# Optimization experiments

Measured on AMD Instinct MI355X. Metric: run time of the kernel, lower is better.

The kernel has to match this reference:

```python
import jax, jax.numpy as jnp
import numpy as np

N, A, C = 65536, 512, 1000


def setup_inputs() -> dict:
    key = jax.random.key(0)
    k1, k2, k3, k4, k5 = jax.random.split(key, 5)
    return {
        "features": jax.random.normal(k1, (N, A), dtype=jnp.float32),
        "labels": jax.random.randint(k2, (N,), 0, C),
        "count": jax.random.uniform(k3, (C,), dtype=jnp.float32) * 100.0,
        "mean": jax.random.normal(k4, (C, A), dtype=jnp.float32),
        "cov": jax.random.uniform(k5, (C, A), dtype=jnp.float32),
    }


def reference(features, labels, count, mean, cov):
    # Per-class counts and feature sums via segment reduction (math identical to
    # the torch onehot-expand NxCxA construction, but O(N*A) instead of O(N*C*A)).
    c = count.shape[0]
    ones = jnp.ones((features.shape[0],), dtype=features.dtype)
    n_c = jax.ops.segment_sum(ones, labels, num_segments=c)            # [C]
    sums = jax.ops.segment_sum(features, labels, num_segments=c)      # [C, A]
    amt = jnp.where(n_c == 0, 1.0, n_c)                                # Amount_CxA (zeros -> 1)
    ave = sums / amt[:, None]                                          # ave_CxA
    diff = features - ave[labels]                                      # onehot*(x - ave) per row
    var = jax.ops.segment_sum(diff * diff, labels, num_segments=c) / amt[:, None]
    # EMA blend weight; torch sets NaN (0/0) entries to 0.
    denom = n_c + count
    w = jnp.where(denom == 0, 0.0, n_c / jnp.where(denom == 0, 1.0, denom))[:, None]  # [C,1]
    cov_new = cov * (1.0 - w) + var * w + w * (1.0 - w) * (mean - ave) ** 2
    mean_new = mean * (1.0 - w) + ave * w
    count_new = count + n_c
    return cov_new, mean_new, count_new
```

## Files before the change

kernel.cpp:

```cpp
#include <hip/hip_runtime.h>
#include <hip/hip_bf16.h>

constexpr int N_ROWS = 65536;
constexpr int N_FEAT = 512;
constexpr int N_FEAT2 = N_FEAT / 2;
constexpr int N_CLS  = 1000;
constexpr int CLS_PAD = 1024;


__global__ void hist_kernel(const int* __restrict__ labels, int* __restrict__ nc, int n) {
    int i = blockIdx.x * blockDim.x + threadIdx.x;
    if (i < n) atomicAdd(&nc[labels[i]], 1);
}

__global__ void scan_kernel(const int* __restrict__ nc,
                            int* __restrict__ offs, int* __restrict__ cursor) {
    __shared__ int tmp[CLS_PAD];
    int t = threadIdx.x;
    int v = (t < N_CLS) ? nc[t] : 0;
    tmp[t] = v;
    __syncthreads();
    for (int d = 1; d < CLS_PAD; d <<= 1) {
        int x = (t >= d) ? tmp[t - d] : 0;
        __syncthreads();
        tmp[t] += x;
        __syncthreads();
    }
    int excl = tmp[t] - v;
    if (t < N_CLS) { offs[t] = excl; cursor[t] = excl; }
}

__global__ void scatter_kernel(const int* __restrict__ labels,
                               int* __restrict__ cursor, int* __restrict__ perm, int n) {
    int i = blockIdx.x * blockDim.x + threadIdx.x;
    if (i < n) {
        int c = labels[i];
        int pos = atomicAdd(&cursor[c], 1);
        perm[pos] = i;
    }
}

__global__ __launch_bounds__(256) void estimator_main(
    const float* __restrict__ features,
    const float* __restrict__ count,
    const float* __restrict__ mean,
    const float* __restrict__ cov,
    const int* __restrict__ nc,
    const int* __restrict__ offs,
    const int* __restrict__ perm,
    float* __restrict__ out) {
    const int c = blockIdx.x;
    const int t = threadIdx.x;
    const int n = nc[c];
    const int start = offs[c];

    __shared__ int lrows[256];
    const float2* __restrict__ f2 = (const float2*)features;

    float sx = 0.f, sy = 0.f, qx = 0.f, qy = 0.f;

    for (int base = 0; base < n; base += 256) {
        int chunk = min(256, n - base);
        __syncthreads();
        if (t < chunk) lrows[t] = perm[start + base + t];
        __syncthreads();
        #pragma unroll 4
        for (int j = 0; j < chunk; ++j) {
            int r = lrows[j];
            float2 v = f2[(size_t)r * N_FEAT2 + t];
            sx += v.x; sy += v.y;
            qx += v.x * v.x; qy += v.y * v.y;
        }
    }

    const float fn  = (float)n;
    const float amt = (n > 0) ? fn : 1.0f;
    const float inv = 1.0f / amt;
    const float avx = sx * inv, avy = sy * inv;
    const float vrx = qx * inv - avx * avx;
    const float vry = qy * inv - avy * avy;

    const float cnt   = count[c];
    const float denom = fn + cnt;
    const float w     = (denom == 0.f) ? 0.f : fn / denom;
    const float omw   = 1.0f - w;

    const float2 mv = ((const float2*)mean)[c * N_FEAT2 + t];
    const float2 cv = ((const float2*)cov)[c * N_FEAT2 + t];
    const float dx = mv.x - avx, dy = mv.y - avy;

    float2 covn, meann;
    covn.x  = cv.x * omw + vrx * w + w * omw * dx * dx;
    covn.y  = cv.y * omw + vry * w + w * omw * dy * dy;
    meann.x = mv.x * omw + avx * w;
    meann.y = mv.y * omw + avy * w;

    float2* outc = (float2*)out;
    float2* outm = (float2*)(out + N_CLS * N_FEAT);
    outc[c * N_FEAT2 + t] = covn;
    outm[c * N_FEAT2 + t] = meann;
    if (t == 0) out[2 * N_CLS * N_FEAT + c] = cnt + fn;
}

extern "C" void kernel_launch(void* const* d_in, const int* in_sizes, int n_in,
                              void* d_out, int out_size, void* d_ws, size_t ws_size,
                              hipStream_t stream) {
    const float* features = (const float*)d_in[0];
    const int*   labels   = (const int*)d_in[1];
    const float* count    = (const float*)d_in[2];
    const float* mean     = (const float*)d_in[3];
    const float* cov      = (const float*)d_in[4];
    float* out = (float*)d_out;

    char* ws = (char*)d_ws;
    int* nc     = (int*)(ws + 0);
    int* offs   = (int*)(ws + 4096);
    int* cursor = (int*)(ws + 8192);
    int* perm   = (int*)(ws + 12288);

    hipMemsetAsync(nc, 0, CLS_PAD * sizeof(int), stream);

    hist_kernel<<<(N_ROWS + 255) / 256, 256, 0, stream>>>(labels, nc, N_ROWS);
    scan_kernel<<<1, CLS_PAD, 0, stream>>>(nc, offs, cursor);
    scatter_kernel<<<(N_ROWS + 255) / 256, 256, 0, stream>>>(labels, cursor, perm, N_ROWS);
    estimator_main<<<N_CLS, 256, 0, stream>>>(features, count, mean, cov,
                                              nc, offs, perm, out);
}
```

Before: 239.5 us.

## Fuse histogram, scan, scatter and estimator into one cooperative kernel

Replaces the memset and four separate kernel launches with a single cooperative kernel that uses grid-wide syncs between the histogram, prefix scan, scatter and per-class reduction phases. The aim is to remove launch overhead and inter-kernel gaps. The trade-off is the cost of four grid barriers, plus the requirement that all 1000 blocks are co-resident; the cooperative launch fails if they are not. The scan now uses 256 threads, each handling four classes.

```diff
diff --git a/kernel.cpp b/kernel.cpp
--- a/kernel.cpp
+++ b/kernel.cpp
@@ -1,72 +1,79 @@
 #include <hip/hip_runtime.h>
-#include <hip/hip_bf16.h>
+#include <hip/hip_cooperative_groups.h>
 
-constexpr int N_ROWS = 65536;
-constexpr int N_FEAT = 512;
+namespace cg = cooperative_groups;
+
+constexpr int N_ROWS  = 65536;
+constexpr int N_FEAT  = 512;
 constexpr int N_FEAT2 = N_FEAT / 2;
-constexpr int N_CLS  = 1000;
-constexpr int CLS_PAD = 1024;
+constexpr int N_CLS   = 1000;
+constexpr int GRID    = 1000;
+constexpr int BLOCK   = 256;
 
 
-__global__ void hist_kernel(const int* __restrict__ labels, int* __restrict__ nc, int n) {
-    int i = blockIdx.x * blockDim.x + threadIdx.x;
-    if (i < n) atomicAdd(&nc[labels[i]], 1);
-}
-
-__global__ void scan_kernel(const int* __restrict__ nc,
-                            int* __restrict__ offs, int* __restrict__ cursor) {
-    __shared__ int tmp[CLS_PAD];
-    int t = threadIdx.x;
-    int v = (t < N_CLS) ? nc[t] : 0;
-    tmp[t] = v;
-    __syncthreads();
-    for (int d = 1; d < CLS_PAD; d <<= 1) {
-        int x = (t >= d) ? tmp[t - d] : 0;
-        __syncthreads();
-        tmp[t] += x;
-        __syncthreads();
-    }
-    int excl = tmp[t] - v;
-    if (t < N_CLS) { offs[t] = excl; cursor[t] = excl; }
-}
-
-__global__ void scatter_kernel(const int* __restrict__ labels,
-                               int* __restrict__ cursor, int* __restrict__ perm, int n) {
-    int i = blockIdx.x * blockDim.x + threadIdx.x;
-    if (i < n) {
-        int c = labels[i];
-        int pos = atomicAdd(&cursor[c], 1);
-        perm[pos] = i;
-    }
-}
-
-__global__ __launch_bounds__(256) void estimator_main(
+__global__ __launch_bounds__(BLOCK) void estimator_all(
     const float* __restrict__ features,
+    const int*   __restrict__ labels,
     const float* __restrict__ count,
     const float* __restrict__ mean,
     const float* __restrict__ cov,
-    const int* __restrict__ nc,
-    const int* __restrict__ offs,
-    const int* __restrict__ perm,
-    float* __restrict__ out) {
-    const int c = blockIdx.x;
-    const int t = threadIdx.x;
+    float*       __restrict__ out,
+    int* __restrict__ nc,
+    int* __restrict__ offs,
+    int* __restrict__ cursor,
+    int* __restrict__ perm)
+{
+    cg::grid_group grid = cg::this_grid();
+    const int b = blockIdx.x, t = threadIdx.x;
+    __shared__ int sh[BLOCK];
+
+    if (b == 0)
+        for (int i = t; i < 1024; i += BLOCK) nc[i] = 0;
+    grid.sync();
+
+    for (int i = b * BLOCK + t; i < N_ROWS; i += GRID * BLOCK)
+        atomicAdd(&nc[labels[i]], 1);
+    grid.sync();
+
+    if (b == 0) {
+        const int i0 = t * 4;
+        int v0 = nc[i0], v1 = nc[i0+1], v2 = nc[i0+2], v3 = nc[i0+3];
+        int s = v0 + v1 + v2 + v3;
+        sh[t] = s;
+        __syncthreads();
+        for (int d = 1; d < BLOCK; d <<= 1) {
+            int x = (t >= d) ? sh[t - d] : 0;
+            __syncthreads();
+            sh[t] += x;
+            __syncthreads();
+        }
+        int o0 = sh[t] - s;
+        int o1 = o0 + v0, o2 = o1 + v1, o3 = o2 + v2;
+        offs[i0] = o0; offs[i0+1] = o1; offs[i0+2] = o2; offs[i0+3] = o3;
+        cursor[i0] = o0; cursor[i0+1] = o1; cursor[i0+2] = o2; cursor[i0+3] = o3;
+    }
+    grid.sync();
+
+    for (int i = b * BLOCK + t; i < N_ROWS; i += GRID * BLOCK) {
+        int c = labels[i];
+        perm[atomicAdd(&cursor[c], 1)] = i;
+    }
+    grid.sync();
+
+    const int c = b;
     const int n = nc[c];
     const int start = offs[c];
-
-    __shared__ int lrows[256];
     const float2* __restrict__ f2 = (const float2*)features;
 
     float sx = 0.f, sy = 0.f, qx = 0.f, qy = 0.f;
-
-    for (int base = 0; base < n; base += 256) {
-        int chunk = min(256, n - base);
+    for (int base = 0; base < n; base += BLOCK) {
+        int chunk = min(BLOCK, n - base);
         __syncthreads();
-        if (t < chunk) lrows[t] = perm[start + base + t];
+        if (t < chunk) sh[t] = perm[start + base + t];
         __syncthreads();
         #pragma unroll 4
         for (int j = 0; j < chunk; ++j) {
-            int r = lrows[j];
+            int r = sh[j];
             float2 v = f2[(size_t)r * N_FEAT2 + t];
             sx += v.x; sy += v.y;
             qx += v.x * v.x; qy += v.y * v.y;
@@ -95,10 +102,8 @@
     meann.x = mv.x * omw + avx * w;
     meann.y = mv.y * omw + avy * w;
 
-    float2* outc = (float2*)out;
-    float2* outm = (float2*)(out + N_CLS * N_FEAT);
-    outc[c * N_FEAT2 + t] = covn;
-    outm[c * N_FEAT2 + t] = meann;
+    ((float2*)out)[c * N_FEAT2 + t] = covn;
+    ((float2*)(out + N_CLS * N_FEAT))[c * N_FEAT2 + t] = meann;
     if (t == 0) out[2 * N_CLS * N_FEAT + c] = cnt + fn;
 }
 
@@ -118,11 +123,8 @@
     int* cursor = (int*)(ws + 8192);
     int* perm   = (int*)(ws + 12288);
 
-    hipMemsetAsync(nc, 0, CLS_PAD * sizeof(int), stream);
-
-    hist_kernel<<<(N_ROWS + 255) / 256, 256, 0, stream>>>(labels, nc, N_ROWS);
-    scan_kernel<<<1, CLS_PAD, 0, stream>>>(nc, offs, cursor);
-    scatter_kernel<<<(N_ROWS + 255) / 256, 256, 0, stream>>>(labels, cursor, perm, N_ROWS);
-    estimator_main<<<N_CLS, 256, 0, stream>>>(features, count, mean, cov,
-                                              nc, offs, perm, out);
+    void* args[] = { &features, &labels, &count, &mean, &cov, &out,
+                     &nc, &offs, &cursor, &perm };
+    hipLaunchCooperativeKernel((const void*)estimator_all,
+                               dim3(GRID), dim3(BLOCK), args, 0, stream);
 }
```

Measured after the change: 575.1 us. 140% more time.

## Fuse histogram and scan into one LDS kernel, vectorize scatter, unroll gathers

Applied to the files above, without the earlier changes.

Replaces the memset, global-atomic histogram and separate scan with a single 1024-thread block that builds the class histogram in shared memory and scans it, deriving counts from consecutive offsets. The scatter kernel now reads labels as int4, with each thread handling four rows. The main gather loop is manually unrolled by eight to keep more independent row loads in flight. The single-block histogram serializes reading the 65536 labels in one workgroup, which may offset the savings from fewer launches.

```diff
diff --git a/kernel.cpp b/kernel.cpp
--- a/kernel.cpp
+++ b/kernel.cpp
@@ -1,43 +1,54 @@
 #include <hip/hip_runtime.h>
-#include <hip/hip_bf16.h>
 
-constexpr int N_ROWS = 65536;
-constexpr int N_FEAT = 512;
+constexpr int N_ROWS  = 65536;
+constexpr int N_FEAT  = 512;
 constexpr int N_FEAT2 = N_FEAT / 2;
-constexpr int N_CLS  = 1000;
-constexpr int CLS_PAD = 1024;
+constexpr int N_CLS   = 1000;
 
 
-__global__ void hist_kernel(const int* __restrict__ labels, int* __restrict__ nc, int n) {
-    int i = blockIdx.x * blockDim.x + threadIdx.x;
-    if (i < n) atomicAdd(&nc[labels[i]], 1);
-}
+__global__ __launch_bounds__(1024) void hist_scan_kernel(
+    const int* __restrict__ labels, int* __restrict__ offs, int* __restrict__ cursor)
+{
+    __shared__ int bins[1024];
+    __shared__ int tmp[1024];
+    const int t = threadIdx.x;
+    bins[t] = 0;
+    __syncthreads();
 
-__global__ void scan_kernel(const int* __restrict__ nc,
-                            int* __restrict__ offs, int* __restrict__ cursor) {
-    __shared__ int tmp[CLS_PAD];
-    int t = threadIdx.x;
-    int v = (t < N_CLS) ? nc[t] : 0;
+    const int4* __restrict__ l4 = (const int4*)labels;
+    #pragma unroll 4
+    for (int i = t; i < N_ROWS / 4; i += 1024) {
+        int4 v = l4[i];
+        atomicAdd(&bins[v.x], 1); atomicAdd(&bins[v.y], 1);
+        atomicAdd(&bins[v.z], 1); atomicAdd(&bins[v.w], 1);
+    }
+    __syncthreads();
+
+    const int v = bins[t];
     tmp[t] = v;
     __syncthreads();
-    for (int d = 1; d < CLS_PAD; d <<= 1) {
+    for (int d = 1; d < 1024; d <<= 1) {
         int x = (t >= d) ? tmp[t - d] : 0;
         __syncthreads();
         tmp[t] += x;
         __syncthreads();
     }
-    int excl = tmp[t] - v;
-    if (t < N_CLS) { offs[t] = excl; cursor[t] = excl; }
+    const int excl = tmp[t] - v;
+    offs[t] = excl;
+    cursor[t] = excl;
+    if (t == 0) offs[1024] = N_ROWS;
 }
 
-__global__ void scatter_kernel(const int* __restrict__ labels,
-                               int* __restrict__ cursor, int* __restrict__ perm, int n) {
-    int i = blockIdx.x * blockDim.x + threadIdx.x;
-    if (i < n) {
-        int c = labels[i];
-        int pos = atomicAdd(&cursor[c], 1);
-        perm[pos] = i;
-    }
+__global__ __launch_bounds__(256) void scatter_kernel(
+    const int* __restrict__ labels, int* __restrict__ cursor, int* __restrict__ perm)
+{
+    const int i = blockIdx.x * blockDim.x + threadIdx.x;
+    const int4 v = ((const int4*)labels)[i];
+    const int r = i * 4;
+    perm[atomicAdd(&cursor[v.x], 1)] = r + 0;
+    perm[atomicAdd(&cursor[v.y], 1)] = r + 1;
+    perm[atomicAdd(&cursor[v.z], 1)] = r + 2;
+    perm[atomicAdd(&cursor[v.w], 1)] = r + 3;
 }
 
 __global__ __launch_bounds__(256) void estimator_main(
@@ -45,31 +56,49 @@
     const float* __restrict__ count,
     const float* __restrict__ mean,
     const float* __restrict__ cov,
-    const int* __restrict__ nc,
     const int* __restrict__ offs,
     const int* __restrict__ perm,
-    float* __restrict__ out) {
+    float* __restrict__ out)
+{
     const int c = blockIdx.x;
     const int t = threadIdx.x;
-    const int n = nc[c];
     const int start = offs[c];
+    const int n = offs[c + 1] - start;
 
-    __shared__ int lrows[256];
+    __shared__ int sh[256];
     const float2* __restrict__ f2 = (const float2*)features;
 
     float sx = 0.f, sy = 0.f, qx = 0.f, qy = 0.f;
 
     for (int base = 0; base < n; base += 256) {
-        int chunk = min(256, n - base);
+        const int chunk = min(256, n - base);
         __syncthreads();
-        if (t < chunk) lrows[t] = perm[start + base + t];
+        if (t < chunk) sh[t] = perm[start + base + t];
         __syncthreads();
-        #pragma unroll 4
-        for (int j = 0; j < chunk; ++j) {
-            int r = lrows[j];
-            float2 v = f2[(size_t)r * N_FEAT2 + t];
-            sx += v.x; sy += v.y;
-            qx += v.x * v.x; qy += v.y * v.y;
+        int j = 0;
+        for (; j + 8 <= chunk; j += 8) {
+            const int r0 = sh[j+0], r1 = sh[j+1], r2 = sh[j+2], r3 = sh[j+3];
+            const int r4 = sh[j+4], r5 = sh[j+5], r6 = sh[j+6], r7 = sh[j+7];
+            const float2 v0 = f2[(size_t)r0 * N_FEAT2 + t];
+            const float2 v1 = f2[(size_t)r1 * N_FEAT2 + t];
+            const float2 v2 = f2[(size_t)r2 * N_FEAT2 + t];
+            const float2 v3 = f2[(size_t)r3 * N_FEAT2 + t];
+            const float2 v4 = f2[(size_t)r4 * N_FEAT2 + t];
+            const float2 v5 = f2[(size_t)r5 * N_FEAT2 + t];
+            const float2 v6 = f2[(size_t)r6 * N_FEAT2 + t];
+            const float2 v7 = f2[(size_t)r7 * N_FEAT2 + t];
+            sx += v0.x; sy += v0.y; qx += v0.x*v0.x; qy += v0.y*v0.y;
+            sx += v1.x; sy += v1.y; qx += v1.x*v1.x; qy += v1.y*v1.y;
+            sx += v2.x; sy += v2.y; qx += v2.x*v2.x; qy += v2.y*v2.y;
+            sx += v3.x; sy += v3.y; qx += v3.x*v3.x; qy += v3.y*v3.y;
+            sx += v4.x; sy += v4.y; qx += v4.x*v4.x; qy += v4.y*v4.y;
+            sx += v5.x; sy += v5.y; qx += v5.x*v5.x; qy += v5.y*v5.y;
+            sx += v6.x; sy += v6.y; qx += v6.x*v6.x; qy += v6.y*v6.y;
+            sx += v7.x; sy += v7.y; qx += v7.x*v7.x; qy += v7.y*v7.y;
+        }
+        for (; j < chunk; ++j) {
+            const float2 v = f2[(size_t)sh[j] * N_FEAT2 + t];
+            sx += v.x; sy += v.y; qx += v.x*v.x; qy += v.y*v.y;
         }
     }
 
@@ -95,10 +124,8 @@
     meann.x = mv.x * omw + avx * w;
     meann.y = mv.y * omw + avy * w;
 
-    float2* outc = (float2*)out;
-    float2* outm = (float2*)(out + N_CLS * N_FEAT);
-    outc[c * N_FEAT2 + t] = covn;
-    outm[c * N_FEAT2 + t] = meann;
+    ((float2*)out)[c * N_FEAT2 + t] = covn;
+    ((float2*)(out + N_CLS * N_FEAT))[c * N_FEAT2 + t] = meann;
     if (t == 0) out[2 * N_CLS * N_FEAT + c] = cnt + fn;
 }
 
@@ -113,16 +140,12 @@
     float* out = (float*)d_out;
 
     char* ws = (char*)d_ws;
-    int* nc     = (int*)(ws + 0);
-    int* offs   = (int*)(ws + 4096);
+    int* offs   = (int*)(ws + 0);
     int* cursor = (int*)(ws + 8192);
     int* perm   = (int*)(ws + 12288);
 
-    hipMemsetAsync(nc, 0, CLS_PAD * sizeof(int), stream);
-
-    hist_kernel<<<(N_ROWS + 255) / 256, 256, 0, stream>>>(labels, nc, N_ROWS);
-    scan_kernel<<<1, CLS_PAD, 0, stream>>>(nc, offs, cursor);
-    scatter_kernel<<<(N_ROWS + 255) / 256, 256, 0, stream>>>(labels, cursor, perm, N_ROWS);
+    hist_scan_kernel<<<1, 1024, 0, stream>>>(labels, offs, cursor);
+    scatter_kernel<<<N_ROWS / 4 / 256, 256, 0, stream>>>(labels, cursor, perm);
     estimator_main<<<N_CLS, 256, 0, stream>>>(features, count, mean, cov,
-                                              nc, offs, perm, out);
+                                              offs, perm, out);
 }
```

Measured after the change: 233.6 us. -2.4%, faster.
